# Optimization experiments

Measured on AMD Instinct MI355X. Metric: run time of the kernel, lower is better.

The kernel has to match this reference:

```python
import jax, jax.numpy as jnp
import numpy as np

B, S, D = 2, 2048, 4096
R, K, H = 4, 8, 128  # kv_repeat, kv heads, head dim (R*K = 32 query heads)


def _rope_tables():
    inv_freq = 1.0 / (10000.0 ** (jnp.arange(0, H, 2, dtype=jnp.float32) / H))  # [H/2]
    freqs = jnp.arange(S, dtype=jnp.float32)[:, None] * inv_freq[None, :]       # [S, H/2]
    emb = jnp.concatenate([freqs, freqs], axis=-1)                              # [S, H]
    return jnp.sin(emb), jnp.cos(emb)


def setup_inputs() -> dict:
    key = jax.random.key(0)
    kx, kq, kk, kv, ko = jax.random.split(key, 5)
    x = jax.random.normal(kx, (B, S, D), dtype=jnp.float32)
    wq = jax.random.normal(kq, (D, R, K, H), dtype=jnp.float32) / jnp.sqrt(jnp.float32(D))
    wk = jax.random.normal(kk, (D, K, H), dtype=jnp.float32) / jnp.sqrt(jnp.float32(D))
    wv = jax.random.normal(kv, (D, K, H), dtype=jnp.float32) / jnp.sqrt(jnp.float32(D))
    wo = jax.random.normal(ko, (R, K, H, D), dtype=jnp.float32) / jnp.sqrt(jnp.float32(R * K * H))
    mask = jnp.triu(jnp.full((S, S), -1e9, dtype=jnp.float32), k=1)  # additive causal mask
    sin, cos = _rope_tables()
    return {"x": x, "wq": wq, "wk": wk, "wv": wv, "wo": wo, "mask": mask, "sin": sin, "cos": cos}


def _rotate_half(t):
    t1, t2 = jnp.split(t, 2, axis=-1)
    return jnp.concatenate([-t2, t1], axis=-1)


def _apply_rope(t, sin, cos):
    # t: [..., S, H]; sin/cos: [S, H] broadcast over leading dims
    return t * cos + _rotate_half(t) * sin


def reference(x, wq, wk, wv, wo, mask, sin, cos):
    # projections: b=batch, s=query seq, t=kv seq, r=kv_repeat, k=kv head, h=head dim
    q = jnp.einsum('bsd,drkh->brksh', x, wq)
    k = jnp.einsum('bsd,dkh->bksh', x, wk)
    v = jnp.einsum('bsd,dkh->bksh', x, wv)
    q = _apply_rope(q, sin, cos)
    k = _apply_rope(k, sin, cos) * (H ** -0.5)  # scale folded into k, as in source
    a = jnp.einsum('brksh,bkth->brkst', q, k) + mask  # [B,R,K,S,S]
    a = jax.nn.softmax(a, axis=-1)
    y = jnp.einsum('brkst,bkth->brksh', a, v)
    return jnp.einsum('brksh,rkhd->bsd', y, wo)
```

## Files before the change

### kernel.cpp

```cpp
#include <hip/hip_runtime.h>

using u16 = unsigned short;
using u32 = unsigned int;

typedef short bf16x8 __attribute__((ext_vector_type(8)));
typedef float f32x4 __attribute__((ext_vector_type(4)));

__device__ __forceinline__ float b2f(u16 u) { return __uint_as_float(((u32)u) << 16); }
__device__ __forceinline__ u16 f2bf(float f) {
  u32 u = __float_as_uint(f);
  u32 r = (u + 0x7fffu + ((u >> 16) & 1u)) >> 16;
  return (u16)r;
}
__device__ __forceinline__ u16 f2bf_trunc(float f) {
  return (u16)(__float_as_uint(f) >> 16);
}

__device__ __forceinline__ void gl16(const u16* g, u16* l) {
  __builtin_amdgcn_global_load_lds((const __attribute__((address_space(1))) u32*)g,
                                   (__attribute__((address_space(3))) u32*)l, 16, 0, 0);
}

__global__ __launch_bounds__(256) void f32_to_bf16_k(const float* __restrict__ in,
                                                     u16* __restrict__ out, int n4) {
  int i = blockIdx.x * 256 + threadIdx.x;
  if (i >= n4) return;
  float4 v = ((const float4*)in)[i];
  ushort4 o;
  o.x = f2bf(v.x); o.y = f2bf(v.y); o.z = f2bf(v.z); o.w = f2bf(v.w);
  ((ushort4*)out)[i] = o;
}

__global__ __launch_bounds__(256) void transpose_to_bf16(const float* __restrict__ in,
                                                         u16* __restrict__ out,
                                                         int Rr, int Cc) {
  __shared__ float tile[32][33];
  const int tx = threadIdx.x;
  const int ty = threadIdx.y;
  const int r0 = blockIdx.y << 5;
  const int c0 = blockIdx.x << 5;
#pragma unroll
  for (int i = 0; i < 4; ++i)
    tile[ty + 8 * i][tx] = in[(size_t)(r0 + ty + 8 * i) * Cc + c0 + tx];
  __syncthreads();
#pragma unroll
  for (int i = 0; i < 4; ++i)
    out[(size_t)(c0 + ty + 8 * i) * Rr + r0 + tx] = f2bf(tile[tx][ty + 8 * i]);
}

#define SWZ4(r) (((r) & 3) ^ (((r) >> 2) & 3))
__global__ __launch_bounds__(256) void gemm128(const u16* __restrict__ A,
                                               const u16* __restrict__ Bt,
                                               void* __restrict__ Cv,
                                               int M, int N, int K, int out_bf16) {
  __shared__ __align__(16) u16 a_t[2 * 128 * 32];
  __shared__ __align__(16) u16 b_t[2 * 128 * 32];
  const int tid = threadIdx.x;
  const int wave = tid >> 6;
  const int lane = tid & 63;
  const int quad = lane >> 4;
  const int l16 = lane & 15;
  const int wm = wave >> 1;
  const int wn = wave & 1;
  const int m0 = blockIdx.y << 7;
  const int n0 = blockIdx.x << 7;

  const int srow = tid >> 2;
  const int scg = ((tid & 3) ^ SWZ4(srow)) << 3;
  const u16* Ag0 = A + (size_t)(m0 + srow) * K + scg;
  const u16* Ag1 = A + (size_t)(m0 + 64 + srow) * K + scg;
  const u16* Bg0 = Bt + (size_t)(n0 + srow) * K + scg;
  const u16* Bg1 = Bt + (size_t)(n0 + 64 + srow) * K + scg;
  u16* al = a_t + wave * 512 + lane * 8;
  u16* bl = b_t + wave * 512 + lane * 8;

  auto stage = [&](int k0, int buf) {
    const int bo = buf * 4096;
    gl16(Ag0 + k0, al + bo);
    gl16(Ag1 + k0, al + bo + 2048);
    gl16(Bg0 + k0, bl + bo);
    gl16(Bg1 + k0, bl + bo + 2048);
  };

  const int fsw = (quad ^ SWZ4(l16)) << 3;
  const u16* afp = a_t + (wm * 64 + l16) * 32 + fsw;
  const u16* bfp = b_t + (wn * 64 + l16) * 32 + fsw;

  f32x4 acc[4][4];
#pragma unroll
  for (int i = 0; i < 4; ++i)
#pragma unroll
    for (int j = 0; j < 4; ++j) acc[i][j] = (f32x4){0.f, 0.f, 0.f, 0.f};

  stage(0, 0);
  int cur = 0;
  for (int k0 = 0; k0 < K; k0 += 32) {
    __syncthreads();
    if (k0 + 32 < K) stage(k0 + 32, cur ^ 1);
    const int bo = cur * 4096;
    bf16x8 af[4], bf[4];
#pragma unroll
    for (int t = 0; t < 4; ++t) {
      af[t] = *(const bf16x8*)(afp + bo + t * 512);
      bf[t] = *(const bf16x8*)(bfp + bo + t * 512);
    }
    __builtin_amdgcn_s_setprio(1);
#pragma unroll
    for (int mt = 0; mt < 4; ++mt)
#pragma unroll
      for (int nt = 0; nt < 4; ++nt)
        acc[mt][nt] = __builtin_amdgcn_mfma_f32_16x16x32_bf16(af[mt], bf[nt], acc[mt][nt], 0, 0, 0);
    __builtin_amdgcn_s_setprio(0);
    cur ^= 1;
  }

  if (out_bf16) {
    u16* C = (u16*)Cv;
#pragma unroll
    for (int mt = 0; mt < 4; ++mt)
#pragma unroll
      for (int r = 0; r < 4; ++r) {
        size_t base = (size_t)(m0 + wm * 64 + mt * 16 + quad * 4 + r) * N + n0 + wn * 64 + l16;
#pragma unroll
        for (int nt = 0; nt < 4; ++nt) C[base + nt * 16] = f2bf(acc[mt][nt][r]);
      }
  } else {
    float* C = (float*)Cv;
#pragma unroll
    for (int mt = 0; mt < 4; ++mt)
#pragma unroll
      for (int r = 0; r < 4; ++r) {
        size_t base = (size_t)(m0 + wm * 64 + mt * 16 + quad * 4 + r) * N + n0 + wn * 64 + l16;
#pragma unroll
        for (int nt = 0; nt < 4; ++nt) C[base + nt * 16] = acc[mt][nt][r];
      }
  }
}

__global__ __launch_bounds__(256) void rope_k_kernel(const u16* __restrict__ kvf,
                                                     u16* __restrict__ kt,
                                                     const float* __restrict__ sinT,
                                                     const float* __restrict__ cosT) {
  int idx = blockIdx.x * 256 + threadIdx.x;
  int h = idx & 127;
  int s = (idx >> 10) & 2047;
  size_t src = (size_t)(idx >> 10) * 2048 + (idx & 1023);
  float t0 = b2f(kvf[src]);
  float tp = b2f(kvf[(h < 64) ? src + 64 : src - 64]);
  float rot = (h < 64) ? -tp : tp;
  float o = (t0 * cosT[(s << 7) + h] + rot * sinT[(s << 7) + h]) * 0.08838834764831845f;
  kt[idx] = f2bf(o);
}

__global__ __launch_bounds__(256) void transpose_v(const u16* __restrict__ kvf,
                                                   u16* __restrict__ vtg) {
  __shared__ u16 tile[32][34];
  const int tx = threadIdx.x;
  const int ty = threadIdx.y;
  const int t0 = blockIdx.x << 5;
  const int h0 = blockIdx.y << 5;
  const int plane = blockIdx.z;
  const int b = plane >> 3, kh = plane & 7;
#pragma unroll
  for (int i = 0; i < 4; ++i) {
    int t = t0 + ty + 8 * i;
    tile[ty + 8 * i][tx] = kvf[(size_t)(b * 2048 + t) * 2048 + 1024 + kh * 128 + h0 + tx];
  }
  __syncthreads();
#pragma unroll
  for (int i = 0; i < 4; ++i)
    vtg[((size_t)plane * 128 + h0 + ty + 8 * i) * 2048 + t0 + tx] = tile[tx][ty + 8 * i];
}

__global__ __launch_bounds__(512, 4) void attn_mfma(const u16* __restrict__ qf,
                                                    const u16* __restrict__ kt,
                                                    const u16* __restrict__ vtg,
                                                    const float* __restrict__ sinT,
                                                    const float* __restrict__ cosT,
                                                    u16* __restrict__ y2) {
  __shared__ __align__(16) u16 kl[2 * 64 * 128];
  __shared__ __align__(16) u16 vt[2 * 128 * 64];
  __shared__ __align__(16) u16 pl[8 * 16 * 64];
  const int tid = threadIdx.x;
  const int wave = tid >> 6;
  const int lane = tid & 63;
  const int quad = lane >> 4;
  const int l16 = lane & 15;
  const int sw7 = l16 & 7;

  const int flat = blockIdx.x | (blockIdx.y << 4) | (blockIdx.z << 9);
  const int kh = flat & 7;
  const int j = flat >> 3;
  const int rep = j & 3;
  const int qt = 15 - ((j >> 2) & 15);
  const int b = j >> 6;
  const int head = (rep << 3) | kh;

  const int qbase = qt << 7;
  const int srow = qbase + wave * 16 + l16;
  const int row_min = qbase + wave * 16;
  const int nchunk = 2 * qt + 2;

  const size_t kbase0 = ((size_t)(b * 2048) * 8 + kh) * 128;
  const size_t vbase0 = ((size_t)(b * 8 + kh)) * 128 * 2048;

  const int krow0 = wave * 8 + (lane >> 4);
  const int krow1 = krow0 + 4;
  const u16* gK0 = kt + kbase0 + (size_t)krow0 * 1024 + (((lane & 15) ^ (krow0 & 7)) << 3);
  const u16* gK1 = kt + kbase0 + (size_t)krow1 * 1024 + (((lane & 15) ^ (krow1 & 7)) << 3);
  const int vrow0 = wave * 16 + (lane >> 3);
  const int vrow1 = vrow0 + 8;
  const u16* gV0 = vtg + vbase0 + (size_t)vrow0 * 2048 + (((lane & 7) ^ (vrow0 & 7)) << 3);
  const u16* gV1 = vtg + vbase0 + (size_t)vrow1 * 2048 + (((lane & 7) ^ (vrow1 & 7)) << 3);

  auto stage = [&](int c, int buf) {
    u16* kd = kl + buf * 8192 + wave * 1024 + lane * 8;
    u16* vd = vt + buf * 8192 + wave * 1024 + lane * 8;
    size_t ko = (size_t)c * 65536;
    size_t vo = (size_t)c * 64;
    gl16(gK0 + ko, kd);
    gl16(gK1 + ko, kd + 512);
    gl16(gV0 + vo, vd);
    gl16(gV1 + vo, vd + 512);
  };

  stage(0, 0);

  bf16x8 qfrag[4];
  {
    size_t base = ((size_t)(b * 2048 + srow)) * 4096 + (size_t)head * 128;
    float qv[32];
#pragma unroll
    for (int kk = 0; kk < 4; ++kk) {
      uint4 w = *(const uint4*)(qf + base + kk * 32 + quad * 8);
      const u16* ws = (const u16*)&w;
#pragma unroll
      for (int jj = 0; jj < 8; ++jj) qv[kk * 8 + jj] = b2f(ws[jj]);
    }
    const float* cp = cosT + (size_t)srow * 128;
    const float* sp = sinT + (size_t)srow * 128;
#pragma unroll
    for (int kk = 0; kk < 2; ++kk) {
      int hb = kk * 32 + quad * 8;
      float4 c0 = *(const float4*)(cp + hb);
      float4 c1 = *(const float4*)(cp + hb + 4);
      float4 s0 = *(const float4*)(sp + hb);
      float4 s1 = *(const float4*)(sp + hb + 4);
      float cc[8] = {c0.x, c0.y, c0.z, c0.w, c1.x, c1.y, c1.z, c1.w};
      float ss[8] = {s0.x, s0.y, s0.z, s0.w, s1.x, s1.y, s1.z, s1.w};
#pragma unroll
      for (int jj = 0; jj < 8; ++jj) {
        float a = qv[kk * 8 + jj];
        float bb = qv[(kk + 2) * 8 + jj];
        qfrag[kk][jj] = (short)f2bf(a * cc[jj] - bb * ss[jj]);
        qfrag[kk + 2][jj] = (short)f2bf(bb * cc[jj] + a * ss[jj]);
      }
    }
  }

  f32x4 o[8];
#pragma unroll
  for (int i = 0; i < 8; ++i) o[i] = (f32x4){0.f, 0.f, 0.f, 0.f};
  float run_m[4] = {-1e30f, -1e30f, -1e30f, -1e30f};
  float run_l[4] = {0.f, 0.f, 0.f, 0.f};

  u16* plw = pl + wave * 1024;
  int cur = 0;

  for (int c = 0; c < nchunk; ++c) {
    __syncthreads();
    if (c + 1 < nchunk) stage(c + 1, cur ^ 1);

    if (c * 64 <= row_min + 15) {
      const u16* kb = kl + cur * 8192;
      const u16* vb = vt + cur * 8192;

      f32x4 s[4];
      __builtin_amdgcn_s_setprio(1);
#pragma unroll
      for (int nt = 0; nt < 4; ++nt) {
        s[nt] = (f32x4){0.f, 0.f, 0.f, 0.f};
#pragma unroll
        for (int kk = 0; kk < 4; ++kk) {
          bf16x8 bf = *(const bf16x8*)(kb + (nt * 16 + l16) * 128 + (((kk * 4 + quad) ^ sw7) << 3));
          s[nt] = __builtin_amdgcn_mfma_f32_16x16x32_bf16(qfrag[kk], bf, s[nt], 0, 0, 0);
        }
      }
      __builtin_amdgcn_s_setprio(0);

      if (c * 64 + 63 > row_min) {
        int rbase = row_min + quad * 4 - c * 64;
#pragma unroll
        for (int nt = 0; nt < 4; ++nt)
#pragma unroll
          for (int rr = 0; rr < 4; ++rr)
            if (nt * 16 + l16 > rbase + rr) s[nt][rr] = -1e30f;
      }

      float p[4][4];
#pragma unroll
      for (int rr = 0; rr < 4; ++rr) {
        float cm = fmaxf(fmaxf(s[0][rr], s[1][rr]), fmaxf(s[2][rr], s[3][rr]));
#pragma unroll
        for (int off = 1; off < 16; off <<= 1) cm = fmaxf(cm, __shfl_xor(cm, off));
        float newm = fmaxf(run_m[rr], cm);
        float alpha = __expf(run_m[rr] - newm);
        float rs = 0.f;
#pragma unroll
        for (int nt = 0; nt < 4; ++nt) {
          float pv = __expf(s[nt][rr] - newm);
          p[nt][rr] = pv;
          rs += pv;
        }
#pragma unroll
        for (int off = 1; off < 16; off <<= 1) rs += __shfl_xor(rs, off);
        run_l[rr] = run_l[rr] * alpha + rs;
        run_m[rr] = newm;
#pragma unroll
        for (int ht = 0; ht < 8; ++ht) o[ht][rr] *= alpha;
      }

#pragma unroll
      for (int nt = 0; nt < 4; ++nt)
#pragma unroll
        for (int rr = 0; rr < 4; ++rr) {
          int prow = quad * 4 + rr;
          plw[prow * 64 + (((nt * 2 + (l16 >> 3)) ^ (prow & 7)) << 3) + (l16 & 7)] =
              f2bf_trunc(p[nt][rr]);
        }

      __builtin_amdgcn_s_setprio(1);
#pragma unroll
      for (int kk = 0; kk < 2; ++kk) {
        bf16x8 af = *(const bf16x8*)(plw + l16 * 64 + (((kk * 4 + quad) ^ sw7) << 3));
#pragma unroll
        for (int ht = 0; ht < 8; ++ht) {
          bf16x8 bf = *(const bf16x8*)(vb + (ht * 16 + l16) * 64 + (((kk * 4 + quad) ^ sw7) << 3));
          o[ht] = __builtin_amdgcn_mfma_f32_16x16x32_bf16(af, bf, o[ht], 0, 0, 0);
        }
      }
      __builtin_amdgcn_s_setprio(0);
    }
    cur ^= 1;
  }

  float inv_l[4];
#pragma unroll
  for (int rr = 0; rr < 4; ++rr) inv_l[rr] = 1.0f / run_l[rr];
#pragma unroll
  for (int rr = 0; rr < 4; ++rr) {
    int row = qbase + wave * 16 + quad * 4 + rr;
    size_t base = ((size_t)(b * 2048 + row)) * 4096 + (size_t)head * 128 + l16;
#pragma unroll
    for (int ht = 0; ht < 8; ++ht)
      y2[base + ht * 16] = f2bf(o[ht][rr] * inv_l[rr]);
  }
}

extern "C" void kernel_launch(void* const* d_in, const int* in_sizes, int n_in,
                              void* d_out, int out_size, void* d_ws, size_t ws_size,
                              hipStream_t stream) {
  const float* x = (const float*)d_in[0];
  const float* wq = (const float*)d_in[1];
  const float* wk = (const float*)d_in[2];
  const float* wv = (const float*)d_in[3];
  const float* wo = (const float*)d_in[4];
  const float* sinT = (const float*)d_in[6];
  const float* cosT = (const float*)d_in[7];
  float* out = (float*)d_out;

  char* ws = (char*)d_ws;
  size_t off = 0;
  auto alloc = [&](size_t bytes) -> void* {
    void* p = ws + off;
    off += (bytes + 255) & ~(size_t)255;
    return p;
  };
  u16* xb  = (u16*)alloc(16777216ull * 2);
  u16* wqT = (u16*)alloc(16777216ull * 2);
  u16* wkT = (u16*)alloc(4194304ull * 2);
  u16* wvT = (u16*)alloc(4194304ull * 2);
  u16* woT = (u16*)alloc(16777216ull * 2);
  u16* qf  = (u16*)alloc(16777216ull * 2);
  u16* kvf = (u16*)alloc(8388608ull * 2);
  u16* ktb = (u16*)alloc(4194304ull * 2);
  u16* y2  = (u16*)alloc(16777216ull * 2);
  (void)wvT;

  dim3 tb(32, 8);
  f32_to_bf16_k<<<dim3(16384), 256, 0, stream>>>(x, xb, 4194304);
  transpose_to_bf16<<<dim3(128, 128), tb, 0, stream>>>(wq, wqT, 4096, 4096);
  transpose_to_bf16<<<dim3(32, 128), tb, 0, stream>>>(wk, wkT, 4096, 1024);
  transpose_to_bf16<<<dim3(32, 128), tb, 0, stream>>>(wv, wvT, 4096, 1024);
  transpose_to_bf16<<<dim3(128, 128), tb, 0, stream>>>(wo, woT, 4096, 4096);

  gemm128<<<dim3(32, 32), 256, 0, stream>>>(xb, wqT, qf, 4096, 4096, 4096, 1);
  gemm128<<<dim3(16, 32), 256, 0, stream>>>(xb, wkT, kvf, 4096, 2048, 4096, 1);

  rope_k_kernel<<<dim3(16384), 256, 0, stream>>>(kvf, ktb, sinT, cosT);

  u16* vtg = wkT;
  transpose_v<<<dim3(64, 4, 16), tb, 0, stream>>>(kvf, vtg);

  attn_mfma<<<dim3(16, 32, 2), 512, 0, stream>>>(qf, ktb, vtg, sinT, cosT, y2);

  gemm128<<<dim3(32, 32), 256, 0, stream>>>(y2, woT, out, 4096, 4096, 4096, 0);
}
```

Measured before the change: 899.6 us.

## Add 256x256-tile pipelined bf16 GEMM for Q and output projections

Adds a new GEMM kernel with 256x256 output tiles and 512 threads. It double-buffers LDS through direct global-to-LDS loads with explicit barrier and vmcnt scheduling, an XOR-swizzled LDS layout, raised MFMA wave priority, and a grouped tile ordering for L2 locality. It replaces the 128-tile GEMM for the 4096x4096x4096 Q projection and output projection. The aim is more operand reuse per LDS byte and overlap of loads with MFMA. In exchange the kernel is hardcoded to 256 blocks with tm/tn derived for a 16x16 tile grid, and its hand-written synchronization is fragile.

Measured after the change: 750.1 us. 1.2x faster.

```diff
diff --git a/kernel.cpp b/kernel.cpp
--- a/kernel.cpp
+++ b/kernel.cpp
@@ -20,6 +20,9 @@
   __builtin_amdgcn_global_load_lds((const __attribute__((address_space(1))) u32*)g,
                                    (__attribute__((address_space(3))) u32*)l, 16, 0, 0);
 }
+
+#define BARF asm volatile("s_barrier" ::: "memory")
+#define VMW4 asm volatile("s_waitcnt vmcnt(4)" ::: "memory")
 
 __global__ __launch_bounds__(256) void f32_to_bf16_k(const float* __restrict__ in,
                                                      u16* __restrict__ out, int n4) {
@@ -137,6 +140,160 @@
   }
 }
 
+__global__ __launch_bounds__(512, 2) void gemm256(const u16* __restrict__ A,
+                                                  const u16* __restrict__ Bt,
+                                                  void* __restrict__ Cv,
+                                                  int N, int K, int out_bf16) {
+  __shared__ __align__(16) u16 lA[2 * 256 * 64];
+  __shared__ __align__(16) u16 lB[2 * 256 * 64];
+  const int tid = threadIdx.x;
+  const int wave = tid >> 6, lane = tid & 63;
+  const int quad = lane >> 4, l16 = lane & 15;
+  const int wr = wave >> 2, wc = wave & 3;
+  const int sw7 = l16 & 7;
+
+  const int x = blockIdx.x;
+  const int wg = (x & 7) * 32 + (x >> 3);
+  const int tm = wg >> 4, tn = wg & 15;
+
+  const int srow = tid >> 3;
+  const int gch = ((tid & 7) ^ (srow & 7)) << 3;
+  const u16* gA0 = A + (size_t)(tm * 256 + srow) * K + gch;
+  const u16* gA1 = A + (size_t)(tm * 256 + 128 + srow) * K + gch;
+  const u16* gB0 = Bt + (size_t)(tn * 256 + srow) * K + gch;
+  const u16* gB1 = Bt + (size_t)(tn * 256 + 128 + srow) * K + gch;
+  const int nkt = (K >> 6) - 1;
+
+  auto stageA = [&](int kt, int h, int buf) {
+    const int kc = (kt <= nkt) ? kt : 0;
+    const u16* g = (h ? gA1 : gA0) + (size_t)kc * 64;
+    u16* d = lA + buf * 16384 + h * 8192 + tid * 8;
+    gl16(g, d);
+    gl16(g + (size_t)K * 64, d + 4096);
+  };
+  auto stageB = [&](int kt, int h, int buf) {
+    const int kc = (kt <= nkt) ? kt : 0;
+    const u16* g = (h ? gB1 : gB0) + (size_t)kc * 64;
+    u16* d = lB + buf * 16384 + h * 8192 + tid * 8;
+    gl16(g, d);
+    gl16(g + (size_t)K * 64, d + 4096);
+  };
+
+  const u16* aLk0 = lA + l16 * 64 + ((quad ^ sw7) << 3);
+  const u16* aLk1 = lA + l16 * 64 + (((4 + quad) ^ sw7) << 3);
+  const u16* bLk0 = lB + l16 * 64 + ((quad ^ sw7) << 3);
+  const u16* bLk1 = lB + l16 * 64 + (((4 + quad) ^ sw7) << 3);
+
+  bf16x8 bA[8], bB0[4], bB1[4];
+  auto loadA = [&](int buf, int rh) {
+    const int ro = buf * 16384 + (wr * 128 + rh * 64) * 64;
+#pragma unroll
+    for (int mt = 0; mt < 4; ++mt) {
+      bA[mt * 2] = *(const bf16x8*)(aLk0 + ro + mt * 1024);
+      bA[mt * 2 + 1] = *(const bf16x8*)(aLk1 + ro + mt * 1024);
+    }
+  };
+  auto loadB0 = [&](int buf, int ch) {
+    const int ro = buf * 16384 + (wc * 64 + ch * 32) * 64;
+#pragma unroll
+    for (int nt = 0; nt < 2; ++nt) {
+      bB0[nt * 2] = *(const bf16x8*)(bLk0 + ro + nt * 1024);
+      bB0[nt * 2 + 1] = *(const bf16x8*)(bLk1 + ro + nt * 1024);
+    }
+  };
+  auto loadB1 = [&](int buf, int ch) {
+    const int ro = buf * 16384 + (wc * 64 + ch * 32) * 64;
+#pragma unroll
+    for (int nt = 0; nt < 2; ++nt) {
+      bB1[nt * 2] = *(const bf16x8*)(bLk0 + ro + nt * 1024);
+      bB1[nt * 2 + 1] = *(const bf16x8*)(bLk1 + ro + nt * 1024);
+    }
+  };
+
+  f32x4 acc[2][2][4][2];
+#pragma unroll
+  for (int a = 0; a < 2; ++a)
+#pragma unroll
+    for (int b = 0; b < 2; ++b)
+#pragma unroll
+      for (int m = 0; m < 4; ++m)
+#pragma unroll
+        for (int n = 0; n < 2; ++n) acc[a][b][m][n] = (f32x4){0.f, 0.f, 0.f, 0.f};
+
+  auto domfma = [&](f32x4(&q)[4][2], const bf16x8(&bB)[4]) {
+    __builtin_amdgcn_s_setprio(1);
+#pragma unroll
+    for (int mt = 0; mt < 4; ++mt)
+#pragma unroll
+      for (int nt = 0; nt < 2; ++nt) {
+        q[mt][nt] = __builtin_amdgcn_mfma_f32_16x16x32_bf16(bA[mt * 2], bB[nt * 2], q[mt][nt], 0, 0, 0);
+        q[mt][nt] = __builtin_amdgcn_mfma_f32_16x16x32_bf16(bA[mt * 2 + 1], bB[nt * 2 + 1], q[mt][nt], 0, 0, 0);
+      }
+    __builtin_amdgcn_s_setprio(0);
+  };
+
+  stageB(0, 0, 0); stageA(0, 0, 0); stageA(0, 1, 0); stageB(0, 1, 0);
+  stageB(1, 0, 1); stageA(1, 0, 1);
+  VMW4;
+  BARF;
+
+  const int niter = K >> 7;
+#pragma unroll 1
+  for (int it = 0; it < niter; ++it) {
+    const int t1 = 2 * it + 1, t2 = 2 * it + 2, t3 = 2 * it + 3;
+    loadA(0, 0); loadB0(0, 0); stageA(t1, 1, 1);
+    BARF; domfma(acc[0][0], bB0); BARF;
+    loadB1(0, 1); stageB(t1, 1, 1);
+    BARF; domfma(acc[0][1], bB1); BARF;
+    loadA(0, 1); stageB(t2, 0, 0);
+    BARF; domfma(acc[1][0], bB0); BARF;
+    stageA(t2, 0, 0); VMW4;
+    BARF; domfma(acc[1][1], bB1); BARF;
+    loadA(1, 0); loadB0(1, 0); stageA(t2, 1, 0);
+    BARF; domfma(acc[0][0], bB0); BARF;
+    loadB1(1, 1); stageB(t2, 1, 0);
+    BARF; domfma(acc[0][1], bB1); BARF;
+    loadA(1, 1); stageB(t3, 0, 1);
+    BARF; domfma(acc[1][0], bB0); BARF;
+    stageA(t3, 0, 1); VMW4;
+    BARF; domfma(acc[1][1], bB1); BARF;
+  }
+
+  if (out_bf16) {
+    u16* C = (u16*)Cv;
+#pragma unroll
+    for (int rh = 0; rh < 2; ++rh)
+#pragma unroll
+      for (int mt = 0; mt < 4; ++mt)
+#pragma unroll
+        for (int r = 0; r < 4; ++r) {
+          size_t base = (size_t)(tm * 256 + wr * 128 + rh * 64 + mt * 16 + quad * 4 + r) * N +
+                        tn * 256 + wc * 64 + l16;
+#pragma unroll
+          for (int ch = 0; ch < 2; ++ch)
+#pragma unroll
+            for (int nt = 0; nt < 2; ++nt)
+              C[base + ch * 32 + nt * 16] = f2bf(acc[rh][ch][mt][nt][r]);
+        }
+  } else {
+    float* C = (float*)Cv;
+#pragma unroll
+    for (int rh = 0; rh < 2; ++rh)
+#pragma unroll
+      for (int mt = 0; mt < 4; ++mt)
+#pragma unroll
+        for (int r = 0; r < 4; ++r) {
+          size_t base = (size_t)(tm * 256 + wr * 128 + rh * 64 + mt * 16 + quad * 4 + r) * N +
+                        tn * 256 + wc * 64 + l16;
+#pragma unroll
+          for (int ch = 0; ch < 2; ++ch)
+#pragma unroll
+            for (int nt = 0; nt < 2; ++nt)
+              C[base + ch * 32 + nt * 16] = acc[rh][ch][mt][nt][r];
+        }
+  }
+}
+
 __global__ __launch_bounds__(256) void rope_k_kernel(const u16* __restrict__ kvf,
                                                      u16* __restrict__ kt,
                                                      const float* __restrict__ sinT,
@@ -394,7 +551,7 @@
   transpose_to_bf16<<<dim3(32, 128), tb, 0, stream>>>(wv, wvT, 4096, 1024);
   transpose_to_bf16<<<dim3(128, 128), tb, 0, stream>>>(wo, woT, 4096, 4096);
 
-  gemm128<<<dim3(32, 32), 256, 0, stream>>>(xb, wqT, qf, 4096, 4096, 4096, 1);
+  gemm256<<<dim3(256), 512, 0, stream>>>(xb, wqT, qf, 4096, 4096, 1);
   gemm128<<<dim3(16, 32), 256, 0, stream>>>(xb, wkT, kvf, 4096, 2048, 4096, 1);
 
   rope_k_kernel<<<dim3(16384), 256, 0, stream>>>(kvf, ktb, sinT, cosT);
@@ -404,5 +561,5 @@
 
   attn_mfma<<<dim3(16, 32, 2), 512, 0, stream>>>(qf, ktb, vtg, sinT, cosT, y2);
 
-  gemm128<<<dim3(32, 32), 256, 0, stream>>>(y2, woT, out, 4096, 4096, 4096, 0);
-}
+  gemm256<<<dim3(256), 512, 0, stream>>>(y2, woT, out, 4096, 4096, 0);
+}
```
